# Kernel optimization log

Measured on AMD Instinct MI355X. Metric: run time of the kernel, lower is better.

## Reference

```python
import jax, jax.numpy as jnp
import numpy as np

# Mamba2 default hyperparameters
D_MODEL = 768
EXPAND = 2
D_STATE = 128
D_CONV = 4
HEADDIM = 64
D_INNER = EXPAND * D_MODEL            # 1536
NHEADS = D_INNER // HEADDIM           # 24
CONV_DIM = D_INNER + 2 * D_STATE      # 1792 (ngroups=1)
D_IN_PROJ = 2 * D_INNER + 2 * D_STATE + NHEADS  # 3352
B = 4
L = 2048
EPS = 1e-5


def setup_inputs() -> dict:
    key = jax.random.key(0)
    ks = jax.random.split(key, 8)
    return {
        "x": jax.random.normal(ks[0], (B, L, D_MODEL), jnp.float32),
        "in_proj_w": jax.random.normal(ks[1], (D_IN_PROJ, D_MODEL), jnp.float32) * 0.02,
        "conv_w": jax.random.normal(ks[2], (CONV_DIM, D_CONV), jnp.float32) * 0.2,
        "conv_b": jnp.zeros((CONV_DIM,), jnp.float32),
        # inverse-softplus of dt in [1e-3, 0.1] (Mamba2 dt init)
        "dt_bias": jnp.log(jnp.expm1(jax.random.uniform(ks[3], (NHEADS,), jnp.float32, 1e-3, 0.1))),
        "A_log": jnp.log(jax.random.uniform(ks[4], (NHEADS,), jnp.float32, 1.0, 16.0)),
        "D": jnp.ones((NHEADS,), jnp.float32),
        "norm_w": jnp.ones((D_INNER,), jnp.float32),
        "out_proj_w": jax.random.normal(ks[5], (D_MODEL, D_INNER), jnp.float32) * 0.02,
    }


def _mamba2(x, in_proj_w, conv_w, conv_b, dt_bias, A_log, D, norm_w, out_proj_w):
    b, l, _ = x.shape
    zxbcdt = x @ in_proj_w.T                              # (b,l,D_IN_PROJ)
    z, xBC, dt = jnp.split(zxbcdt, [D_INNER, D_INNER + CONV_DIM], axis=-1)

    # causal depthwise conv1d over channels of xBC, kernel D_CONV
    xp = jnp.pad(xBC, ((0, 0), (D_CONV - 1, 0), (0, 0)))
    conv = conv_b + sum(xp[:, k:k + l, :] * conv_w[:, k] for k in range(D_CONV))
    xBC = jax.nn.silu(conv)

    xh, Bm, Cm = jnp.split(xBC, [D_INNER, D_INNER + D_STATE], axis=-1)
    xh = xh.reshape(b, l, NHEADS, HEADDIM)               # (b,l,h,p)

    dt = jax.nn.softplus(dt + dt_bias)                   # (b,l,h)
    A = -jnp.exp(A_log)                                  # (h,)
    dA = jnp.exp(dt * A)                                 # (b,l,h)

    # selective SSM scan over time (state: (b,h,p,n))
    def step(state, inp):
        dA_t, dt_t, x_t, B_t, C_t = inp
        state = state * dA_t[:, :, None, None] \
              + (dt_t[:, :, None] * x_t)[..., None] * B_t[:, None, None, :]
        y_t = jnp.einsum('bhpn,bn->bhp', state, C_t)
        return state, y_t

    state0 = jnp.zeros((b, NHEADS, HEADDIM, D_STATE), x.dtype)
    xs = (dA.transpose(1, 0, 2), dt.transpose(1, 0, 2),
          xh.transpose(1, 0, 2, 3), Bm.transpose(1, 0, 2), Cm.transpose(1, 0, 2))
    _, ys = jax.lax.scan(step, state0, xs)               # (l,b,h,p)
    y = ys.transpose(1, 0, 2, 3) + D[:, None] * xh       # D skip connection
    y = y.reshape(b, l, D_INNER)

    # gated RMSNorm (norm_before_gate=False): normalize after gating by silu(z)
    y = y * jax.nn.silu(z)
    y = y * jax.lax.rsqrt(jnp.mean(y * y, axis=-1, keepdims=True) + EPS) * norm_w
    return y @ out_proj_w.T


def reference(x, in_proj_w, conv_w, conv_b, dt_bias, A_log, D, norm_w, out_proj_w):
    # MambaBlock.forward: Mamba2(x) + x
    return _mamba2(x, in_proj_w, conv_w, conv_b, dt_bias, A_log, D, norm_w, out_proj_w) + x
```

## Files before the change

### kernel.cpp

```cpp
#include <hip/hip_runtime.h>
#include <math.h>

typedef __bf16 bf16x8 __attribute__((ext_vector_type(8)));
typedef float  f32x4  __attribute__((ext_vector_type(4)));

#define QCHUNK 128
#define NCHUNK 16
#define SLD 136

__device__ __forceinline__ float bf2f(unsigned short u) {
    union { unsigned int i; float f; } v; v.i = ((unsigned int)u) << 16; return v.f;
}
__device__ __forceinline__ unsigned short f2bf(float f) {
    union { float f; unsigned int i; } v; v.f = f;
    unsigned int x = v.i;
    unsigned int r = (x + 0x7FFFu + ((x >> 16) & 1u)) >> 16;
    return (unsigned short)r;
}
__device__ __forceinline__ uint4 pack8(float4 a, float4 b) {
    uint4 r;
    r.x = (unsigned)f2bf(a.x) | ((unsigned)f2bf(a.y) << 16);
    r.y = (unsigned)f2bf(a.z) | ((unsigned)f2bf(a.w) << 16);
    r.z = (unsigned)f2bf(b.x) | ((unsigned)f2bf(b.y) << 16);
    r.w = (unsigned)f2bf(b.z) | ((unsigned)f2bf(b.w) << 16);
    return r;
}
__device__ __forceinline__ void load_lds16(const void* g, void* l) {
    __builtin_amdgcn_global_load_lds((const __attribute__((address_space(1))) void*)g,
                                     (__attribute__((address_space(3))) void*)l,
                                     16, 0, 0);
}

__global__ __launch_bounds__(256)
void convert_kernel(const float* __restrict__ x, const float* __restrict__ w_in,
                    const float* __restrict__ w_out,
                    unsigned short* __restrict__ x_bf, unsigned short* __restrict__ w_in_bf,
                    unsigned short* __restrict__ w_out_bf) {
    int idx = blockIdx.x * 256 + threadIdx.x;
    const int NX  = 8192 * 768 / 8;
    const int NW1 = 3328 * 768 / 8;
    const int NW2 = 768 * 1536 / 8;
    if (idx < NX) {
        const float* s = x + (size_t)idx * 8;
        *(uint4*)(x_bf + (size_t)idx * 8) = pack8(*(const float4*)s, *(const float4*)(s + 4));
    } else if (idx < NX + NW1) {
        int j = idx - NX;
        const float* s = w_in + (size_t)j * 8;
        *(uint4*)(w_in_bf + (size_t)j * 8) = pack8(*(const float4*)s, *(const float4*)(s + 4));
    } else if (idx < NX + NW1 + NW2) {
        int j = idx - NX - NW1;
        const float* s = w_out + (size_t)j * 8;
        *(uint4*)(w_out_bf + (size_t)j * 8) = pack8(*(const float4*)s, *(const float4*)(s + 4));
    }
}

__global__ __launch_bounds__(512)
void gemm_8phase(const unsigned short* __restrict__ A,
                 const unsigned short* __restrict__ Bw,
                 unsigned short* __restrict__ Out,
                 int ldo, int K) {
    extern __shared__ __align__(16) char smem[];

    const int tid = threadIdx.x;
    const int bid = blockIdx.x;
    const int xcd = bid & 7, local = bid >> 3;
    const int mt = xcd * 4 + local / 13;
    const int nt = local % 13;
    const int m0 = mt * 256, n0 = nt * 256;

    const int wave = tid >> 6, lane = tid & 63;
    const int wr = wave >> 2, wc = wave & 3;
    const int lr = lane & 15, q = lane >> 4;

    const int gl   = (lr & 7) << 4;
    const int arow = wr * 128 + lr;
    const int brow = wc * 64 + lr;
    const int colq = q << 4;

    const int srow  = tid >> 3;
    const int sslot = (tid & 7) ^ (srow & 7);
    const unsigned short* ga = A  + (size_t)(m0 + srow) * K + sslot * 8;
    const unsigned short* gb = Bw + (size_t)(n0 + srow) * K + sslot * 8;
    char* sAd = smem +         (size_t)tid * 16;
    char* sBd = smem + 65536 + (size_t)tid * 16;
    const size_t gstep = (size_t)64 * K;

    const int NT = K >> 6;
    f32x4 acc[8][4] = {};

    #pragma unroll
    for (int i = 0; i < 4; ++i) {
        load_lds16(ga + (size_t)i * gstep, sAd + i * 8192);
        load_lds16(gb + (size_t)i * gstep, sBd + i * 8192);
    }

    for (int t = 0; t < NT; ++t) {
        const int d = t & 1;
        const bool more = (t + 1 < NT);
        if (more) {
            const size_t kg = (size_t)(t + 1) * 64;
            const int ld = (d ^ 1) * 32768;
            #pragma unroll
            for (int i = 0; i < 4; ++i) {
                load_lds16(ga + kg + (size_t)i * gstep, sAd + ld + i * 8192);
                load_lds16(gb + kg + (size_t)i * gstep, sBd + ld + i * 8192);
            }
            asm volatile("s_waitcnt vmcnt(8)" ::: "memory");
        } else {
            asm volatile("s_waitcnt vmcnt(0)" ::: "memory");
        }
        __builtin_amdgcn_s_barrier();

        const char* pa = smem +         d * 32768;
        const char* pb = smem + 65536 + d * 32768;
        #pragma unroll
        for (int kh = 0; kh < 2; ++kh) {
            const int col = ((kh << 6) | colq) ^ gl;
            bf16x8 af[8], bfr[4];
            #pragma unroll
            for (int m = 0; m < 8; ++m)
                af[m] = *(const bf16x8*)(pa + (arow + m * 16) * 128 + col);
            #pragma unroll
            for (int n = 0; n < 4; ++n)
                bfr[n] = *(const bf16x8*)(pb + (brow + n * 16) * 128 + col);

            __builtin_amdgcn_s_setprio(1);
            #pragma unroll
            for (int m = 0; m < 8; ++m)
                #pragma unroll
                for (int n = 0; n < 4; ++n)
                    acc[m][n] = __builtin_amdgcn_mfma_f32_16x16x32_bf16(af[m], bfr[n], acc[m][n], 0, 0, 0);
            __builtin_amdgcn_s_setprio(0);
        }
        __builtin_amdgcn_s_barrier();
    }

    #pragma unroll
    for (int m = 0; m < 8; ++m) {
        #pragma unroll
        for (int r = 0; r < 4; ++r) {
            int row = m0 + wr * 128 + m * 16 + q * 4 + r;
            #pragma unroll
            for (int n = 0; n < 4; ++n) {
                int col = n0 + wc * 64 + n * 16 + lr;
                Out[(size_t)row * ldo + col] = f2bf(acc[m][n][r]);
            }
        }
    }
}

__global__ __launch_bounds__(512)
void gemm_out(const unsigned short* __restrict__ A,
              const unsigned short* __restrict__ Bw,
              float* __restrict__ Out, const float* __restrict__ Resid,
              int lda) {
    extern __shared__ __align__(16) char smem[];
    const int K = 1536, Nn = 768;

    const int tid = threadIdx.x;
    const int bid = blockIdx.x;
    const int xcd = bid & 7, local = bid >> 3;
    const int mt = xcd * 8 + local / 6;
    const int nt = local % 6;
    const int m0 = mt * 128, n0 = nt * 128;

    const int wave = tid >> 6, lane = tid & 63;
    const int wr = wave >> 2, wc = wave & 3;
    const int lr = lane & 15, q = lane >> 4;

    const int gl   = (lr & 7) << 4;
    const int arow = wr * 64 + lr;
    const int brow = wc * 32 + lr;
    const int colq = q << 4;

    const int srow  = tid >> 3;
    const int sslot = (tid & 7) ^ (srow & 7);
    const unsigned short* ga = A  + (size_t)(m0 + srow) * lda + sslot * 8;
    const unsigned short* gb = Bw + (size_t)(n0 + srow) * K   + sslot * 8;
    char* sAd = smem +         (size_t)tid * 16;
    char* sBd = smem + 32768 + (size_t)tid * 16;
    const size_t gstep_a = (size_t)64 * lda;
    const size_t gstep_b = (size_t)64 * K;

    f32x4 acc[4][2] = {};

    #pragma unroll
    for (int i = 0; i < 2; ++i) {
        load_lds16(ga + (size_t)i * gstep_a, sAd + i * 8192);
        load_lds16(gb + (size_t)i * gstep_b, sBd + i * 8192);
    }

    const int NT = K >> 6;
    for (int t = 0; t < NT; ++t) {
        const int d = t & 1;
        const bool more = (t + 1 < NT);
        if (more) {
            const size_t kg = (size_t)(t + 1) * 64;
            const int ld = (d ^ 1) * 16384;
            #pragma unroll
            for (int i = 0; i < 2; ++i) {
                load_lds16(ga + kg + (size_t)i * gstep_a, sAd + ld + i * 8192);
                load_lds16(gb + kg + (size_t)i * gstep_b, sBd + ld + i * 8192);
            }
            asm volatile("s_waitcnt vmcnt(4)" ::: "memory");
        } else {
            asm volatile("s_waitcnt vmcnt(0)" ::: "memory");
        }
        __builtin_amdgcn_s_barrier();

        const char* pa = smem +         d * 16384;
        const char* pb = smem + 32768 + d * 16384;
        #pragma unroll
        for (int kh = 0; kh < 2; ++kh) {
            const int col = ((kh << 6) | colq) ^ gl;
            bf16x8 af[4], bfr[2];
            #pragma unroll
            for (int m = 0; m < 4; ++m)
                af[m] = *(const bf16x8*)(pa + (arow + m * 16) * 128 + col);
            #pragma unroll
            for (int n = 0; n < 2; ++n)
                bfr[n] = *(const bf16x8*)(pb + (brow + n * 16) * 128 + col);

            __builtin_amdgcn_s_setprio(1);
            #pragma unroll
            for (int m = 0; m < 4; ++m)
                #pragma unroll
                for (int n = 0; n < 2; ++n)
                    acc[m][n] = __builtin_amdgcn_mfma_f32_16x16x32_bf16(af[m], bfr[n], acc[m][n], 0, 0, 0);
            __builtin_amdgcn_s_setprio(0);
        }
        __builtin_amdgcn_s_barrier();
    }

    #pragma unroll
    for (int m = 0; m < 4; ++m) {
        #pragma unroll
        for (int r = 0; r < 4; ++r) {
            int row = m0 + wr * 64 + m * 16 + q * 4 + r;
            #pragma unroll
            for (int n = 0; n < 2; ++n) {
                int col = n0 + wc * 32 + n * 16 + lr;
                Out[(size_t)row * Nn + col] = acc[m][n][r] + Resid[(size_t)row * Nn + col];
            }
        }
    }
}

__global__ __launch_bounds__(256)
void conv_fused_kernel(const unsigned short* __restrict__ zx,
                       const float* __restrict__ cw, const float* __restrict__ cb,
                       unsigned short* __restrict__ xT, unsigned short* __restrict__ bT,
                       unsigned short* __restrict__ Brow, unsigned short* __restrict__ Crow) {
    __shared__ unsigned short outt[64][66];
    __shared__ float cwl[64][4];
    __shared__ float cbl[64];

    int blk = blockIdx.x;
    int cht = blk % 28;
    int tt  = (blk / 28) % 32;
    int b   = blk / (28 * 32);
    int ch0 = cht * 64, t0 = tt * 64;
    int tid = threadIdx.x;
    int tx = tid & 63, ty = tid >> 6;

    if (tid < 64) cbl[tid] = cb[ch0 + tid];
    cwl[tid >> 2][tid & 3] = cw[(ch0 + (tid >> 2)) * 4 + (tid & 3)];
    __syncthreads();

    const unsigned short* zp = zx + (size_t)(b * 2048) * 3352 + 1536 + ch0 + tx;
    float w0 = cwl[tx][0], w1 = cwl[tx][1], w2 = cwl[tx][2], w3 = cwl[tx][3];
    float bias = cbl[tx];
    int tg = t0 + ty * 16;
    float r0 = (tg >= 3) ? bf2f(zp[(size_t)(tg - 3) * 3352]) : 0.f;
    float r1 = (tg >= 2) ? bf2f(zp[(size_t)(tg - 2) * 3352]) : 0.f;
    float r2 = (tg >= 1) ? bf2f(zp[(size_t)(tg - 1) * 3352]) : 0.f;
    #pragma unroll
    for (int k = 0; k < 16; ++k) {
        float cur = bf2f(zp[(size_t)(tg + k) * 3352]);
        float a = bias + r0 * w0 + r1 * w1 + r2 * w2 + cur * w3;
        a = a / (1.f + expf(-a));
        outt[ty * 16 + k][tx] = f2bf(a);
        r0 = r1; r1 = r2; r2 = cur;
    }
    __syncthreads();

    if (ch0 < 1536) {
        unsigned short* dst = xT + ((size_t)(b * 1536 + ch0)) * 2048 + t0;
        #pragma unroll
        for (int k = 0; k < 16; ++k) {
            int chl = ty * 16 + k;
            dst[(size_t)chl * 2048 + tx] = outt[tx][chl];
        }
    } else if (ch0 < 1664) {
        int n0 = ch0 - 1536;
        unsigned short* dstT = bT + ((size_t)(b * 128 + n0)) * 2048 + t0;
        #pragma unroll
        for (int k = 0; k < 16; ++k) {
            int chl = ty * 16 + k;
            dstT[(size_t)chl * 2048 + tx] = outt[tx][chl];
        }
        unsigned short* dstR = Brow + ((size_t)(b * 2048 + t0)) * 128 + n0;
        int tl = tid >> 3, c8 = (tid & 7) << 3;
        #pragma unroll
        for (int it = 0; it < 2; ++it) {
            int t = tl + it * 32;
            unsigned short tmp[8];
            #pragma unroll
            for (int jj = 0; jj < 8; ++jj) tmp[jj] = outt[t][c8 + jj];
            *(uint4*)(dstR + (size_t)t * 128 + c8) = *(uint4*)tmp;
        }
    } else {
        int n0 = ch0 - 1664;
        unsigned short* dstR = Crow + ((size_t)(b * 2048 + t0)) * 128 + n0;
        int tl = tid >> 3, c8 = (tid & 7) << 3;
        #pragma unroll
        for (int it = 0; it < 2; ++it) {
            int t = tl + it * 32;
            unsigned short tmp[8];
            #pragma unroll
            for (int jj = 0; jj < 8; ++jj) tmp[jj] = outt[t][c8 + jj];
            *(uint4*)(dstR + (size_t)t * 128 + c8) = *(uint4*)tmp;
        }
    }
}

__global__ __launch_bounds__(256)
void dt_kernel(const float* __restrict__ x, const float* __restrict__ w_in,
               const float* __restrict__ dt_bias, const float* __restrict__ A_log,
               float2* __restrict__ dtdA) {
    __shared__ float xs[8 * 768];
    __shared__ float wsh[24 * 257];
    const int tid = threadIdx.x;
    const int row0 = blockIdx.x * 8;

    for (int i = tid; i < 8 * 768 / 4; i += 256)
        *(float4*)(xs + i * 4) = *(const float4*)(x + (size_t)row0 * 768 + (size_t)i * 4);

    const int rr = tid / 24, hh = tid - rr * 24;
    float acc0 = 0.f, acc1 = 0.f, acc2 = 0.f, acc3 = 0.f;

    for (int kc = 0; kc < 3; ++kc) {
        __syncthreads();
        for (int i = tid; i < 24 * 256; i += 256) {
            int h = i >> 8, kk = i & 255;
            wsh[h * 257 + kk] = w_in[(size_t)(3328 + h) * 768 + kc * 256 + kk];
        }
        __syncthreads();
        if (tid < 192) {
            const float* xp = xs + rr * 768 + kc * 256;
            const float* wp = wsh + hh * 257;
            #pragma unroll 16
            for (int kk = 0; kk < 256; kk += 4) {
                acc0 += xp[kk]     * wp[kk];
                acc1 += xp[kk + 1] * wp[kk + 1];
                acc2 += xp[kk + 2] * wp[kk + 2];
                acc3 += xp[kk + 3] * wp[kk + 3];
            }
        }
    }
    if (tid < 192) {
        float v = (acc0 + acc1) + (acc2 + acc3) + dt_bias[hh];
        float dt = (v > 20.f) ? v : log1pf(expf(v));
        float A = -expf(A_log[hh]);
        dtdA[(size_t)(row0 + rr) * 24 + hh] = make_float2(dt, dt * A);
    }
}

__global__ __launch_bounds__(256)
void ssd_local_kernel(const unsigned short* __restrict__ Brow,
                      const unsigned short* __restrict__ Crow,
                      const float2* __restrict__ dtdA,
                      const unsigned short* __restrict__ xT,
                      const unsigned short* __restrict__ bT,
                      const float* __restrict__ Dh,
                      unsigned short* __restrict__ yb,
                      unsigned short* __restrict__ sst,
                      float* __restrict__ Pbuf) {
    extern __shared__ __align__(16) char smem[];
    __bf16* Bs  = (__bf16*)smem;
    __bf16* Cs  = (__bf16*)(smem + 34816);
    float*  Lc  = (float*)(smem + 69632);
    float*  dtl = (float*)(smem + 70144);

    const int tid = threadIdx.x;
    const int c   = blockIdx.x & 15;
    const int bh  = blockIdx.x >> 4;
    const int b   = bh / 24, h = bh % 24;
    const int t0g = b * 2048 + c * QCHUNK;
    const int wave = tid >> 6, lane = tid & 63;
    const int lr = lane & 15, q = lane >> 4;

    for (int cc = tid; cc < 2048; cc += 256) {
        int r = cc >> 4, c8 = (cc & 15) << 3;
        *(uint4*)(Bs + r * SLD + c8) = *(const uint4*)(Brow + ((size_t)(t0g + r)) * 128 + c8);
        *(uint4*)(Cs + r * SLD + c8) = *(const uint4*)(Crow + ((size_t)(t0g + r)) * 128 + c8);
    }
    if (tid < 128) {
        float2 dd = dtdA[((size_t)t0g + tid) * 24 + h];
        dtl[tid] = dd.x;
        Lc[tid]  = dd.y;
    }
    __syncthreads();
    if (tid < 64) {
        float a0 = Lc[2 * tid], a1 = Lc[2 * tid + 1];
        float s = a0 + a1;
        #pragma unroll
        for (int d = 1; d < 64; d <<= 1) {
            float v = __shfl_up(s, d);
            if (tid >= d) s += v;
        }
        float ex = s - (a0 + a1);
        Lc[2 * tid]     = ex + a0;
        Lc[2 * tid + 1] = ex + a0 + a1;
    }
    __syncthreads();

    const int wm = (wave & 1) * 64, wn = (wave >> 1) * 64;
    f32x4 g[4][4] = {};
    #pragma unroll
    for (int k0 = 0; k0 < 128; k0 += 32) {
        bf16x8 af[4], bfr[4];
        #pragma unroll
        for (int t = 0; t < 4; ++t) {
            af[t]  = *(const bf16x8*)(Cs + (wm + t * 16 + lr) * SLD + k0 + q * 8);
            bfr[t] = *(const bf16x8*)(Bs + (wn + t * 16 + lr) * SLD + k0 + q * 8);
        }
        #pragma unroll
        for (int ti = 0; ti < 4; ++ti)
            #pragma unroll
            for (int tj = 0; tj < 4; ++tj)
                g[ti][tj] = __builtin_amdgcn_mfma_f32_16x16x32_bf16(af[ti], bfr[tj], g[ti][tj], 0, 0, 0);
    }
    __syncthreads();

    __bf16* Ms = Cs;
    {
        float lt_[4], dt_[4];
        #pragma unroll
        for (int tj = 0; tj < 4; ++tj) {
            int tau = wn + tj * 16 + lr;
            lt_[tj] = Lc[tau];
            dt_[tj] = dtl[tau];
        }
        #pragma unroll
        for (int ti = 0; ti < 4; ++ti) {
            #pragma unroll
            for (int r = 0; r < 4; ++r) {
                int t = wm + ti * 16 + q * 4 + r;
                float Lt = Lc[t];
                #pragma unroll
                for (int tj = 0; tj < 4; ++tj) {
                    int tau = wn + tj * 16 + lr;
                    float mv = (tau <= t) ? g[ti][tj][r] * expf(Lt - lt_[tj]) * dt_[tj] : 0.f;
                    unsigned short u = f2bf(mv);
                    Ms[t * SLD + tau] = *(__bf16*)&u;
                }
            }
        }
    }

    __bf16* Xt  = Bs;
    __bf16* Xtw = (__bf16*)(smem + 17408);
    {
        float LQ = Lc[127];
        const unsigned short* xTb = xT + ((size_t)(b * 1536 + h * 64)) * 2048 + c * QCHUNK;
        for (int cc = tid; cc < 1024; cc += 256) {
            int p = cc >> 4, c8 = (cc & 15) << 3;
            uint4 v = *(const uint4*)(xTb + (size_t)p * 2048 + c8);
            *(uint4*)(Xt + p * SLD + c8) = v;
            unsigned short uu[8] = {(unsigned short)(v.x & 0xFFFF), (unsigned short)(v.x >> 16),
                                    (unsigned short)(v.y & 0xFFFF), (unsigned short)(v.y >> 16),
                                    (unsigned short)(v.z & 0xFFFF), (unsigned short)(v.z >> 16),
                                    (unsigned short)(v.w & 0xFFFF), (unsigned short)(v.w >> 16)};
            float w0[8];
            #pragma unroll
            for (int jj = 0; jj < 8; ++jj) {
                int tau = c8 + jj;
                w0[jj] = bf2f(uu[jj]) * expf(LQ - Lc[tau]) * dtl[tau];
            }
            *(uint4*)(Xtw + p * SLD + c8) = pack8(make_float4(w0[0], w0[1], w0[2], w0[3]),
                                                  make_float4(w0[4], w0[5], w0[6], w0[7]));
        }
    }
    __syncthreads();

    {
        f32x4 so[2][4] = {};
        const unsigned short* bTb = bT + ((size_t)(b * 128)) * 2048 + c * QCHUNK;
        #pragma unroll
        for (int k0 = 0; k0 < 128; k0 += 32) {
            bf16x8 af[2], bfr[4];
            #pragma unroll
            for (int ti = 0; ti < 2; ++ti) {
                int n = wave * 32 + ti * 16 + lr;
                af[ti] = *(const bf16x8*)(bTb + (size_t)n * 2048 + k0 + q * 8);
            }
            #pragma unroll
            for (int tj = 0; tj < 4; ++tj)
                bfr[tj] = *(const bf16x8*)(Xtw + (tj * 16 + lr) * SLD + k0 + q * 8);
            #pragma unroll
            for (int ti = 0; ti < 2; ++ti)
                #pragma unroll
                for (int tj = 0; tj < 4; ++tj)
                    so[ti][tj] = __builtin_amdgcn_mfma_f32_16x16x32_bf16(af[ti], bfr[tj], so[ti][tj], 0, 0, 0);
        }
        unsigned short* sb = sst + ((size_t)(bh * NCHUNK + c)) * 8192;
        #pragma unroll
        for (int ti = 0; ti < 2; ++ti) {
            #pragma unroll
            for (int r = 0; r < 4; ++r) {
                int n = wave * 32 + ti * 16 + q * 4 + r;
                #pragma unroll
                for (int tj = 0; tj < 4; ++tj) {
                    int p = tj * 16 + lr;
                    sb[n * 64 + p] = f2bf(so[ti][tj][r]);
                }
            }
        }
        if (tid == 0) Pbuf[bh * NCHUNK + c] = expf(Lc[127]);
    }

    {
        f32x4 ya[2][4] = {};
        #pragma unroll
        for (int k0 = 0; k0 < 128; k0 += 32) {
            bf16x8 af[2], bfr[4];
            #pragma unroll
            for (int ti = 0; ti < 2; ++ti)
                af[ti] = *(const bf16x8*)(Ms + (wave * 32 + ti * 16 + lr) * SLD + k0 + q * 8);
            #pragma unroll
            for (int tj = 0; tj < 4; ++tj)
                bfr[tj] = *(const bf16x8*)(Xt + (tj * 16 + lr) * SLD + k0 + q * 8);
            #pragma unroll
            for (int ti = 0; ti < 2; ++ti)
                #pragma unroll
                for (int tj = 0; tj < 4; ++tj)
                    ya[ti][tj] = __builtin_amdgcn_mfma_f32_16x16x32_bf16(af[ti], bfr[tj], ya[ti][tj], 0, 0, 0);
        }
        float Dv = Dh[h];
        unsigned short* ybb = yb + (size_t)t0g * 1536 + h * 64;
        #pragma unroll
        for (int ti = 0; ti < 2; ++ti) {
            #pragma unroll
            for (int r = 0; r < 4; ++r) {
                int t = wave * 32 + ti * 16 + q * 4 + r;
                #pragma unroll
                for (int tj = 0; tj < 4; ++tj) {
                    int p = tj * 16 + lr;
                    __bf16 xb = Xt[p * SLD + t];
                    float xv = bf2f(*(unsigned short*)&xb);
                    ybb[(size_t)t * 1536 + p] = f2bf(ya[ti][tj][r] + Dv * xv);
                }
            }
        }
    }
}

__global__ __launch_bounds__(256)
void combine_kernel(const unsigned short* __restrict__ sst,
                    unsigned short* __restrict__ sstT,
                    const float* __restrict__ Pbuf) {
    __shared__ unsigned short tl[32 * 130];
    const int blk = blockIdx.x;
    const int bh = blk >> 1;
    const int ph = (blk & 1) * 32;
    const int tid = threadIdx.x;
    const int pl = tid & 31;
    const int nb = tid >> 5;
    const unsigned short* sb = sst + (size_t)bh * NCHUNK * 8192;
    unsigned short* tb = sstT + (size_t)bh * NCHUNK * 8192 + ph * 128;
    const float* Pb = Pbuf + bh * NCHUNK;

    float s[16];
    #pragma unroll
    for (int i = 0; i < 16; ++i) s[i] = 0.f;

    for (int c = 0; c < NCHUNK; ++c) {
        const float Pc = Pb[c];
        const unsigned short* sc = sb + (size_t)c * 8192;
        #pragma unroll
        for (int i = 0; i < 16; ++i) {
            int n = nb + 8 * i;
            unsigned short v = sc[n * 64 + ph + pl];
            tl[pl * 130 + n] = f2bf(s[i]);
            s[i] = Pc * s[i] + bf2f(v);
        }
        __syncthreads();
        uint* tlw = (uint*)tl;
        uint4* tc4 = (uint4*)(tb + (size_t)c * 8192);
        #pragma unroll
        for (int k = 0; k < 2; ++k) {
            int j = tid + k * 256;
            int pp = j >> 4;
            int w0 = pp * 65 + (j & 15) * 4;
            tc4[j] = make_uint4(tlw[w0], tlw[w0 + 1], tlw[w0 + 2], tlw[w0 + 3]);
        }
        __syncthreads();
    }
}

__global__ __launch_bounds__(256)
void ssd_inter_kernel(const unsigned short* __restrict__ Crow,
                      const float2* __restrict__ dtdA,
                      const unsigned short* __restrict__ sstT,
                      unsigned short* __restrict__ yb) {
    __shared__ __align__(16) __bf16 Cs[128 * SLD];
    __shared__ __align__(16) __bf16 St[64 * SLD];
    __shared__ float Lc[128];

    const int tid = threadIdx.x;
    const int blk = blockIdx.x;
    const int bh = blk / 15;
    const int c  = blk % 15 + 1;
    const int b = bh / 24, h = bh % 24;
    const int t0g = b * 2048 + c * QCHUNK;
    const int wave = tid >> 6, lane = tid & 63;
    const int lr = lane & 15, q = lane >> 4;

    for (int cc = tid; cc < 2048; cc += 256) {
        int r = cc >> 4, c8 = (cc & 15) << 3;
        *(uint4*)(Cs + r * SLD + c8) = *(const uint4*)(Crow + ((size_t)(t0g + r)) * 128 + c8);
    }
    const unsigned short* stb = sstT + ((size_t)(bh * NCHUNK + c)) * 8192;
    for (int cc = tid; cc < 1024; cc += 256) {
        int p = cc >> 4, c8 = (cc & 15) << 3;
        *(uint4*)(St + p * SLD + c8) = *(const uint4*)(stb + p * 128 + c8);
    }
    if (tid < 128) Lc[tid] = dtdA[((size_t)t0g + tid) * 24 + h].y;
    __syncthreads();
    if (tid < 64) {
        float a0 = Lc[2 * tid], a1 = Lc[2 * tid + 1];
        float s = a0 + a1;
        #pragma unroll
        for (int d = 1; d < 64; d <<= 1) {
            float v = __shfl_up(s, d);
            if (tid >= d) s += v;
        }
        float ex = s - (a0 + a1);
        Lc[2 * tid]     = ex + a0;
        Lc[2 * tid + 1] = ex + a0 + a1;
    }
    __syncthreads();

    f32x4 ya[2][4] = {};
    #pragma unroll
    for (int k0 = 0; k0 < 128; k0 += 32) {
        bf16x8 af[2], bfr[4];
        #pragma unroll
        for (int ti = 0; ti < 2; ++ti)
            af[ti] = *(const bf16x8*)(Cs + (wave * 32 + ti * 16 + lr) * SLD + k0 + q * 8);
        #pragma unroll
        for (int tj = 0; tj < 4; ++tj)
            bfr[tj] = *(const bf16x8*)(St + (tj * 16 + lr) * SLD + k0 + q * 8);
        #pragma unroll
        for (int ti = 0; ti < 2; ++ti)
            #pragma unroll
            for (int tj = 0; tj < 4; ++tj)
                ya[ti][tj] = __builtin_amdgcn_mfma_f32_16x16x32_bf16(af[ti], bfr[tj], ya[ti][tj], 0, 0, 0);
    }
    unsigned short* ybb = yb + (size_t)t0g * 1536 + h * 64;
    #pragma unroll
    for (int ti = 0; ti < 2; ++ti) {
        #pragma unroll
        for (int r = 0; r < 4; ++r) {
            int t = wave * 32 + ti * 16 + q * 4 + r;
            float sc = expf(Lc[t]);
            #pragma unroll
            for (int tj = 0; tj < 4; ++tj) {
                int p = tj * 16 + lr;
                unsigned short* yp = ybb + (size_t)t * 1536 + p;
                *yp = f2bf(bf2f(*yp) + sc * ya[ti][tj][r]);
            }
        }
    }
}

__global__ __launch_bounds__(256)
void norm_kernel(const unsigned short* __restrict__ yb,
                 unsigned short* __restrict__ zx,
                 const float* __restrict__ nw) {
    int row = blockIdx.x;
    const unsigned short* yr = yb + (size_t)row * 1536;
    unsigned short* zr = zx + (size_t)row * 3352;
    int tid = threadIdx.x;
    float u[6];
    float ss = 0.f;
    #pragma unroll
    for (int i = 0; i < 6; ++i) {
        int c = tid + i * 256;
        float z = bf2f(zr[c]);
        float uu = bf2f(yr[c]) * (z / (1.f + expf(-z)));
        u[i] = uu;
        ss += uu * uu;
    }
    #pragma unroll
    for (int m = 1; m < 64; m <<= 1) ss += __shfl_xor(ss, m);
    __shared__ float red[4];
    if ((tid & 63) == 0) red[tid >> 6] = ss;
    __syncthreads();
    float tot = red[0] + red[1] + red[2] + red[3];
    float inv = rsqrtf(tot * (1.f / 1536.f) + 1e-5f);
    #pragma unroll
    for (int i = 0; i < 6; ++i) {
        int c = tid + i * 256;
        zr[1536 + c] = f2bf(u[i] * inv * nw[c]);
    }
}

extern "C" void kernel_launch(void* const* d_in, const int* in_sizes, int n_in,
                              void* d_out, int out_size, void* d_ws, size_t ws_size,
                              hipStream_t stream) {
    const float* x       = (const float*)d_in[0];
    const float* w_in    = (const float*)d_in[1];
    const float* conv_w  = (const float*)d_in[2];
    const float* conv_b  = (const float*)d_in[3];
    const float* dt_bias = (const float*)d_in[4];
    const float* A_log   = (const float*)d_in[5];
    const float* Dp      = (const float*)d_in[6];
    const float* nw      = (const float*)d_in[7];
    const float* w_out   = (const float*)d_in[8];
    float* out = (float*)d_out;

    char* ws = (char*)d_ws;
    const size_t off_zx   = 0;
    const size_t off_A    = off_zx + 54919168;
    const size_t off_xT   = off_A;
    const size_t off_bT   = off_A + 25165824;
    const size_t off_Brow = off_A + 27262976;
    const size_t off_Crow = off_A + 29360128;
    const size_t off_dtdA = off_A + 58720256;
    const size_t off_y    = off_dtdA + 1572864;
    const size_t off_sst  = off_y + 50331648;
    const size_t off_P    = off_sst + 25165824;

    unsigned short* zx   = (unsigned short*)(ws + off_zx);
    unsigned short* xT   = (unsigned short*)(ws + off_xT);
    unsigned short* bT   = (unsigned short*)(ws + off_bT);
    unsigned short* Brow = (unsigned short*)(ws + off_Brow);
    unsigned short* Crow = (unsigned short*)(ws + off_Crow);
    float2* dtdA = (float2*)(ws + off_dtdA);
    unsigned short* yb   = (unsigned short*)(ws + off_y);
    unsigned short* sst  = (unsigned short*)(ws + off_sst);
    unsigned short* sstT = xT;
    float* Pbuf = (float*)(ws + off_P);

    unsigned short* x_bf     = (unsigned short*)(ws + off_y);
    unsigned short* w_out_bf = (unsigned short*)(ws + off_y + 25165824);
    unsigned short* w_in_bf  = (unsigned short*)(ws + off_sst);

    static bool attr_set = false;
    if (!attr_set) {
        hipFuncSetAttribute((const void*)ssd_local_kernel,
                            hipFuncAttributeMaxDynamicSharedMemorySize, 70656);
        hipFuncSetAttribute((const void*)gemm_8phase,
                            hipFuncAttributeMaxDynamicSharedMemorySize, 131072);
        hipFuncSetAttribute((const void*)gemm_out,
                            hipFuncAttributeMaxDynamicSharedMemorySize, 65536);
        attr_set = true;
    }

    convert_kernel<<<4896, 256, 0, stream>>>(x, w_in, w_out, x_bf, w_in_bf, w_out_bf);
    gemm_8phase<<<416, 512, 131072, stream>>>(x_bf, w_in_bf, zx, 3352, 768);
    conv_fused_kernel<<<3584, 256, 0, stream>>>(zx, conv_w, conv_b, xT, bT, Brow, Crow);
    dt_kernel<<<1024, 256, 0, stream>>>(x, w_in, dt_bias, A_log, dtdA);
    ssd_local_kernel<<<1536, 256, 70656, stream>>>(Brow, Crow, dtdA, xT, bT, Dp, yb, sst, Pbuf);
    combine_kernel<<<192, 256, 0, stream>>>(sst, sstT, Pbuf);
    ssd_inter_kernel<<<1440, 256, 0, stream>>>(Crow, dtdA, sstT, yb);
    norm_kernel<<<8192, 256, 0, stream>>>(yb, zx, nw);
    gemm_out<<<384, 512, 65536, stream>>>(zx + 1536, w_out_bf, out, x, 3352);
}
```

Baseline: 328.8 us.

## Fuse chunk-state combine into inter-chunk SSD kernel, dropping transposed state buffer

Merges combine_kernel and ssd_inter_kernel into one kernel with one block per (batch, head, half of headdim). Each block carries the running inter-chunk state in registers, writes it transposed straight into shared memory, and runs the C·state MFMA for each chunk in sequence. This removes the global round trip through the sstT buffer and one kernel launch. In exchange the grid shrinks from 1440 blocks to 192, and the 15 chunks are handled serially inside each block, so parallelism and latency hiding drop.

```diff
diff --git a/kernel.cpp b/kernel.cpp
--- a/kernel.cpp
+++ b/kernel.cpp
@@ -557,119 +557,102 @@
 }
 
 __global__ __launch_bounds__(256)
-void combine_kernel(const unsigned short* __restrict__ sst,
-                    unsigned short* __restrict__ sstT,
-                    const float* __restrict__ Pbuf) {
-    __shared__ unsigned short tl[32 * 130];
+void ssd_inter_kernel(const unsigned short* __restrict__ Crow,
+                      const float2* __restrict__ dtdA,
+                      const unsigned short* __restrict__ sst,
+                      const float* __restrict__ Pbuf,
+                      unsigned short* __restrict__ yb) {
+    __shared__ __align__(16) __bf16 Cs[128 * SLD];
+    __shared__ __align__(16) __bf16 St[32 * SLD];
+    __shared__ float LcA[15][128];
+
+    const int tid = threadIdx.x;
     const int blk = blockIdx.x;
     const int bh = blk >> 1;
     const int ph = (blk & 1) * 32;
-    const int tid = threadIdx.x;
-    const int pl = tid & 31;
-    const int nb = tid >> 5;
+    const int b = bh / 24, h = bh % 24;
+    const int wave = tid >> 6, lane = tid & 63;
+    const int lr = lane & 15, q = lane >> 4;
+    const int pl = tid & 31, nb = tid >> 5;
+
+    #pragma unroll
+    for (int j = 0; j < 4; ++j) {
+        int cc = 1 + wave + 4 * j;
+        if (cc <= 15) {
+            int tb = b * 2048 + cc * 128;
+            float a0 = dtdA[(size_t)(tb + 2 * lane) * 24 + h].y;
+            float a1 = dtdA[(size_t)(tb + 2 * lane + 1) * 24 + h].y;
+            float s = a0 + a1;
+            #pragma unroll
+            for (int d = 1; d < 64; d <<= 1) {
+                float v = __shfl_up(s, d);
+                if (lane >= d) s += v;
+            }
+            float ex = s - (a0 + a1);
+            LcA[cc - 1][2 * lane]     = ex + a0;
+            LcA[cc - 1][2 * lane + 1] = ex + a0 + a1;
+        }
+    }
+
     const unsigned short* sb = sst + (size_t)bh * NCHUNK * 8192;
-    unsigned short* tb = sstT + (size_t)bh * NCHUNK * 8192 + ph * 128;
     const float* Pb = Pbuf + bh * NCHUNK;
 
     float s[16];
     #pragma unroll
     for (int i = 0; i < 16; ++i) s[i] = 0.f;
 
-    for (int c = 0; c < NCHUNK; ++c) {
+    for (int c = 0; c < 15; ++c) {
         const float Pc = Pb[c];
         const unsigned short* sc = sb + (size_t)c * 8192;
         #pragma unroll
         for (int i = 0; i < 16; ++i) {
             int n = nb + 8 * i;
-            unsigned short v = sc[n * 64 + ph + pl];
-            tl[pl * 130 + n] = f2bf(s[i]);
-            s[i] = Pc * s[i] + bf2f(v);
+            s[i] = Pc * s[i] + bf2f(sc[n * 64 + ph + pl]);
         }
         __syncthreads();
-        uint* tlw = (uint*)tl;
-        uint4* tc4 = (uint4*)(tb + (size_t)c * 8192);
-        #pragma unroll
-        for (int k = 0; k < 2; ++k) {
-            int j = tid + k * 256;
-            int pp = j >> 4;
-            int w0 = pp * 65 + (j & 15) * 4;
-            tc4[j] = make_uint4(tlw[w0], tlw[w0 + 1], tlw[w0 + 2], tlw[w0 + 3]);
+        #pragma unroll
+        for (int i = 0; i < 16; ++i) {
+            int n = nb + 8 * i;
+            unsigned short u = f2bf(s[i]);
+            St[pl * SLD + n] = *(__bf16*)&u;
+        }
+        const int t0g = b * 2048 + (c + 1) * QCHUNK;
+        for (int cc2 = tid; cc2 < 2048; cc2 += 256) {
+            int r = cc2 >> 4, c8 = (cc2 & 15) << 3;
+            *(uint4*)(Cs + r * SLD + c8) = *(const uint4*)(Crow + ((size_t)(t0g + r)) * 128 + c8);
         }
         __syncthreads();
-    }
-}
-
-__global__ __launch_bounds__(256)
-void ssd_inter_kernel(const unsigned short* __restrict__ Crow,
-                      const float2* __restrict__ dtdA,
-                      const unsigned short* __restrict__ sstT,
-                      unsigned short* __restrict__ yb) {
-    __shared__ __align__(16) __bf16 Cs[128 * SLD];
-    __shared__ __align__(16) __bf16 St[64 * SLD];
-    __shared__ float Lc[128];
-
-    const int tid = threadIdx.x;
-    const int blk = blockIdx.x;
-    const int bh = blk / 15;
-    const int c  = blk % 15 + 1;
-    const int b = bh / 24, h = bh % 24;
-    const int t0g = b * 2048 + c * QCHUNK;
-    const int wave = tid >> 6, lane = tid & 63;
-    const int lr = lane & 15, q = lane >> 4;
-
-    for (int cc = tid; cc < 2048; cc += 256) {
-        int r = cc >> 4, c8 = (cc & 15) << 3;
-        *(uint4*)(Cs + r * SLD + c8) = *(const uint4*)(Crow + ((size_t)(t0g + r)) * 128 + c8);
-    }
-    const unsigned short* stb = sstT + ((size_t)(bh * NCHUNK + c)) * 8192;
-    for (int cc = tid; cc < 1024; cc += 256) {
-        int p = cc >> 4, c8 = (cc & 15) << 3;
-        *(uint4*)(St + p * SLD + c8) = *(const uint4*)(stb + p * 128 + c8);
-    }
-    if (tid < 128) Lc[tid] = dtdA[((size_t)t0g + tid) * 24 + h].y;
-    __syncthreads();
-    if (tid < 64) {
-        float a0 = Lc[2 * tid], a1 = Lc[2 * tid + 1];
-        float s = a0 + a1;
-        #pragma unroll
-        for (int d = 1; d < 64; d <<= 1) {
-            float v = __shfl_up(s, d);
-            if (tid >= d) s += v;
-        }
-        float ex = s - (a0 + a1);
-        Lc[2 * tid]     = ex + a0;
-        Lc[2 * tid + 1] = ex + a0 + a1;
-    }
-    __syncthreads();
-
-    f32x4 ya[2][4] = {};
-    #pragma unroll
-    for (int k0 = 0; k0 < 128; k0 += 32) {
-        bf16x8 af[2], bfr[4];
-        #pragma unroll
-        for (int ti = 0; ti < 2; ++ti)
-            af[ti] = *(const bf16x8*)(Cs + (wave * 32 + ti * 16 + lr) * SLD + k0 + q * 8);
-        #pragma unroll
-        for (int tj = 0; tj < 4; ++tj)
-            bfr[tj] = *(const bf16x8*)(St + (tj * 16 + lr) * SLD + k0 + q * 8);
-        #pragma unroll
-        for (int ti = 0; ti < 2; ++ti)
-            #pragma unroll
-            for (int tj = 0; tj < 4; ++tj)
-                ya[ti][tj] = __builtin_amdgcn_mfma_f32_16x16x32_bf16(af[ti], bfr[tj], ya[ti][tj], 0, 0, 0);
-    }
-    unsigned short* ybb = yb + (size_t)t0g * 1536 + h * 64;
-    #pragma unroll
-    for (int ti = 0; ti < 2; ++ti) {
-        #pragma unroll
-        for (int r = 0; r < 4; ++r) {
-            int t = wave * 32 + ti * 16 + q * 4 + r;
-            float sc = expf(Lc[t]);
-            #pragma unroll
-            for (int tj = 0; tj < 4; ++tj) {
-                int p = tj * 16 + lr;
-                unsigned short* yp = ybb + (size_t)t * 1536 + p;
-                *yp = f2bf(bf2f(*yp) + sc * ya[ti][tj][r]);
+
+        f32x4 ya[2][2] = {};
+        #pragma unroll
+        for (int k0 = 0; k0 < 128; k0 += 32) {
+            bf16x8 af[2], bfr[2];
+            #pragma unroll
+            for (int ti = 0; ti < 2; ++ti)
+                af[ti] = *(const bf16x8*)(Cs + (wave * 32 + ti * 16 + lr) * SLD + k0 + q * 8);
+            #pragma unroll
+            for (int tj = 0; tj < 2; ++tj)
+                bfr[tj] = *(const bf16x8*)(St + (tj * 16 + lr) * SLD + k0 + q * 8);
+            #pragma unroll
+            for (int ti = 0; ti < 2; ++ti)
+                #pragma unroll
+                for (int tj = 0; tj < 2; ++tj)
+                    ya[ti][tj] = __builtin_amdgcn_mfma_f32_16x16x32_bf16(af[ti], bfr[tj], ya[ti][tj], 0, 0, 0);
+        }
+        unsigned short* ybb = yb + (size_t)t0g * 1536 + h * 64 + ph;
+        const float* Lcc = LcA[c];
+        #pragma unroll
+        for (int ti = 0; ti < 2; ++ti) {
+            #pragma unroll
+            for (int r = 0; r < 4; ++r) {
+                int t = wave * 32 + ti * 16 + q * 4 + r;
+                float sc2 = expf(Lcc[t]);
+                #pragma unroll
+                for (int tj = 0; tj < 2; ++tj) {
+                    int p = tj * 16 + lr;
+                    unsigned short* yp = ybb + (size_t)t * 1536 + p;
+                    *yp = f2bf(bf2f(*yp) + sc2 * ya[ti][tj][r]);
+                }
             }
         }
     }
@@ -741,7 +724,6 @@
     float2* dtdA = (float2*)(ws + off_dtdA);
     unsigned short* yb   = (unsigned short*)(ws + off_y);
     unsigned short* sst  = (unsigned short*)(ws + off_sst);
-    unsigned short* sstT = xT;
     float* Pbuf = (float*)(ws + off_P);
 
     unsigned short* x_bf     = (unsigned short*)(ws + off_y);
@@ -764,8 +746,7 @@
     conv_fused_kernel<<<3584, 256, 0, stream>>>(zx, conv_w, conv_b, xT, bT, Brow, Crow);
     dt_kernel<<<1024, 256, 0, stream>>>(x, w_in, dt_bias, A_log, dtdA);
     ssd_local_kernel<<<1536, 256, 70656, stream>>>(Brow, Crow, dtdA, xT, bT, Dp, yb, sst, Pbuf);
-    combine_kernel<<<192, 256, 0, stream>>>(sst, sstT, Pbuf);
-    ssd_inter_kernel<<<1440, 256, 0, stream>>>(Crow, dtdA, sstT, yb);
+    ssd_inter_kernel<<<192, 256, 0, stream>>>(Crow, dtdA, sst, Pbuf, yb);
     norm_kernel<<<8192, 256, 0, stream>>>(yb, zx, nw);
     gemm_out<<<384, 512, 65536, stream>>>(zx + 1536, w_out_bf, out, x, 3352);
 }
```

New measurement: 361.9 us. +10.0%, slower.
